# Kernel optimization log

Measured on AMD Instinct MI355X. Metric: run time of the kernel, lower is better.

The kernel has to match this reference:

```python
import jax, jax.numpy as jnp
import numpy as np

N_NODES = 100000
N_EDGES = 1200000
IN_F = 64
OUT_F = 64


def setup_inputs() -> dict:
    key = jax.random.key(0)
    ks = jax.random.split(key, 8)
    rows = jax.random.randint(ks[0], (N_EDGES,), 0, N_NODES)
    cols = jax.random.randint(ks[1], (N_EDGES,), 0, N_NODES)
    vals = jax.random.uniform(ks[2], (N_EDGES,), dtype=jnp.float32)
    features = jax.random.normal(ks[3], (N_NODES, IN_F), dtype=jnp.float32)
    W1 = jax.random.normal(ks[4], (IN_F, OUT_F), dtype=jnp.float32) / np.sqrt(IN_F)
    b1 = jax.random.normal(ks[5], (OUT_F,), dtype=jnp.float32) * 0.01
    W2 = jax.random.normal(ks[6], (IN_F, OUT_F), dtype=jnp.float32) / np.sqrt(IN_F)
    b2 = jax.random.normal(ks[7], (OUT_F,), dtype=jnp.float32) * 0.01
    return {"rows": rows, "cols": cols, "vals": vals, "features": features,
            "W1": W1, "b1": b1, "W2": W2, "b2": b2}


def _spmm(rows, cols, vals, x):
    # y[r] = sum_{e: rows[e]==r} vals[e] * x[cols[e]]  -- COO SpMM via gather + segment_sum
    msgs = vals[:, None] * x[cols]  # [E, F]
    return jax.ops.segment_sum(msgs, rows, num_segments=N_NODES)


def reference(rows, cols, vals, features, W1, b1, W2, b2):
    # L1 = laplacian + selfLoop(identity)  =>  L1 @ X = L @ X + X
    agg1 = _spmm(rows, cols, vals, features) + features          # [N, inF]
    inter_feature = features * features                           # elementwise square
    agg2 = _spmm(rows, cols, vals, inter_feature)                 # [N, inF]
    part1 = agg1 @ W1 + b1                                        # linear
    part2 = agg2 @ W2 + b2                                        # interActTransform
    return part1 + part2
```

## Files before the change

kernel.cpp:

```cpp
#include <hip/hip_runtime.h>


#define ROWS_PER_BUCKET 128
#define ROW_SHIFT 7
#define NBUCK_PAD 784
#define SCAN_T 196
#define CAP 2048
#define CHUNK 4096
#define MAXB 2048
#define COL_BITS 17
#define COL_MASK 0x1FFFF
#define OVF_CAP 65536

typedef __attribute__((ext_vector_type(8))) short bf16x8;
typedef __attribute__((ext_vector_type(4))) float f32x4;

__device__ __forceinline__ unsigned short f2bf(float x) {
    unsigned u = __float_as_uint(x);
    unsigned r = (u + 0x7FFFu + ((u >> 16) & 1u)) >> 16;
    return (unsigned short)r;
}
__device__ __forceinline__ float bf2f(unsigned short h) {
    return __uint_as_float(((unsigned)h) << 16);
}

__global__ __launch_bounds__(256) void node_transform(
    const float* __restrict__ X, const float* __restrict__ W1,
    const float* __restrict__ b1, const float* __restrict__ W2,
    const float* __restrict__ b2, unsigned short* __restrict__ Yb,
    float* __restrict__ Z, int n_nodes,
    int* __restrict__ gcursor, int* __restrict__ ovf_count)
{
    const int tid = threadIdx.x;

    if (gcursor) {
        int gi = blockIdx.x * 256 + tid;
        if (gi < NBUCK_PAD) gcursor[gi] = gi * CAP;
        if (gi == 0) *ovf_count = 0;
    }

    const int lane = tid & 63;
    const int wave = tid >> 6;
    const int lg = lane >> 4;
    const int lr = lane & 15;

    const int base = blockIdx.x * 128 + wave * 32;

    bf16x8 bw1[2][4];
    bf16x8 bw2[2][4];
#pragma unroll
    for (int ks = 0; ks < 2; ++ks) {
#pragma unroll
        for (int cf = 0; cf < 4; ++cf) {
            const int col = cf * 16 + lr;
            const int k0 = ks * 32 + lg * 8;
            bf16x8 t1, t2;
#pragma unroll
            for (int j = 0; j < 8; ++j) {
                t1[j] = (short)f2bf(W1[(k0 + j) * 64 + col]);
                t2[j] = (short)f2bf(W2[(k0 + j) * 64 + col]);
            }
            bw1[ks][cf] = t1;
            bw2[ks][cf] = t2;
        }
    }

    f32x4 acc1[2][4];
    f32x4 acc2[2][4];
#pragma unroll
    for (int rf = 0; rf < 2; ++rf)
#pragma unroll
        for (int cf = 0; cf < 4; ++cf) {
            acc1[rf][cf] = (f32x4){0.f, 0.f, 0.f, 0.f};
            acc2[rf][cf] = (f32x4){0.f, 0.f, 0.f, 0.f};
        }

#pragma unroll
    for (int rf = 0; rf < 2; ++rf) {
        const int row = base + rf * 16 + lr;
        const bool rok = row < n_nodes;
        const float* xp = X + (size_t)row * 64 + lg * 8;
#pragma unroll
        for (int ks = 0; ks < 2; ++ks) {
            float xv[8];
            if (rok) {
                float4 v0 = *(const float4*)(xp + ks * 32);
                float4 v1 = *(const float4*)(xp + ks * 32 + 4);
                xv[0] = v0.x; xv[1] = v0.y; xv[2] = v0.z; xv[3] = v0.w;
                xv[4] = v1.x; xv[5] = v1.y; xv[6] = v1.z; xv[7] = v1.w;
            } else {
#pragma unroll
                for (int j = 0; j < 8; ++j) xv[j] = 0.f;
            }
            bf16x8 a, q;
#pragma unroll
            for (int j = 0; j < 8; ++j) {
                a[j] = (short)f2bf(xv[j]);
                float s = xv[j] * xv[j];
                q[j] = (short)f2bf(s);
            }
#pragma unroll
            for (int cf = 0; cf < 4; ++cf) {
                acc1[rf][cf] = __builtin_amdgcn_mfma_f32_16x16x32_bf16(
                    a, bw1[ks][cf], acc1[rf][cf], 0, 0, 0);
                acc2[rf][cf] = __builtin_amdgcn_mfma_f32_16x16x32_bf16(
                    q, bw2[ks][cf], acc2[rf][cf], 0, 0, 0);
            }
        }
    }

    float bsv[4];
#pragma unroll
    for (int cf = 0; cf < 4; ++cf)
        bsv[cf] = b1[cf * 16 + lr] + b2[cf * 16 + lr];

#pragma unroll
    for (int rf = 0; rf < 2; ++rf) {
#pragma unroll
        for (int i = 0; i < 4; ++i) {
            const int row = base + rf * 16 + lg * 4 + i;
            if (row < n_nodes) {
#pragma unroll
                for (int cf = 0; cf < 4; ++cf) {
                    const float v1 = acc1[rf][cf][i];
                    const float y = v1 + acc2[rf][cf][i];
                    const float z = v1 + bsv[cf];
                    Yb[(size_t)row * 64 + cf * 16 + lr] = f2bf(y);
                    Z[(size_t)row * 64 + cf * 16 + lr] = z;
                }
            }
        }
    }
}


__global__ __launch_bounds__(256) void bin_scatter(
    const int* __restrict__ rows, const int* __restrict__ cols,
    const float* __restrict__ vals, int* __restrict__ gcursor,
    int2* __restrict__ packed, int* __restrict__ ovf_count,
    int4* __restrict__ ovf, int n_edges) {
    __shared__ int lcount[NBUCK_PAD];
    __shared__ int lstart[NBUCK_PAD];
    __shared__ int lcursor[NBUCK_PAD];
    __shared__ int gbase[NBUCK_PAD];
    __shared__ int sx[CHUNK];
    __shared__ int sy[CHUNK];
    __shared__ unsigned short sbk[CHUNK];

    int tid = threadIdx.x;
    int eb0 = blockIdx.x * CHUNK;
    int cnt = min(CHUNK, n_edges - eb0);

    for (int k = tid; k < NBUCK_PAD; k += 256) lcount[k] = 0;
    __syncthreads();

    for (int i = tid; i < cnt; i += 256)
        atomicAdd(&lcount[rows[eb0 + i] >> ROW_SHIFT], 1);
    __syncthreads();

    int c0 = 0, c1 = 0, c2 = 0, c3 = 0, psum = 0;
    if (tid < SCAN_T) {
        c0 = lcount[tid * 4 + 0]; c1 = lcount[tid * 4 + 1];
        c2 = lcount[tid * 4 + 2]; c3 = lcount[tid * 4 + 3];
        psum = c0 + c1 + c2 + c3;
    }
    sx[tid] = psum;
    __syncthreads();
#pragma unroll
    for (int o = 1; o < 256; o <<= 1) {
        int t = (tid >= o) ? sx[tid - o] : 0;
        __syncthreads();
        sx[tid] += t;
        __syncthreads();
    }
    int base0 = sx[tid] - psum;
    __syncthreads();
    if (tid < SCAN_T) {
        lstart[tid * 4 + 0] = base0;
        lstart[tid * 4 + 1] = base0 + c0;
        lstart[tid * 4 + 2] = base0 + c0 + c1;
        lstart[tid * 4 + 3] = base0 + c0 + c1 + c2;
    }
    __syncthreads();

    for (int k = tid; k < NBUCK_PAD; k += 256) {
        lcursor[k] = lstart[k];
        if (lcount[k] > 0) gbase[k] = atomicAdd(&gcursor[k], lcount[k]);
    }
    __syncthreads();

    for (int i = tid; i < cnt; i += 256) {
        int r = rows[eb0 + i];
        int b = r >> ROW_SHIFT;
        int p = atomicAdd(&lcursor[b], 1);
        sx[p] = ((r & (ROWS_PER_BUCKET - 1)) << COL_BITS) | cols[eb0 + i];
        sy[p] = __float_as_int(vals[eb0 + i]);
        sbk[p] = (unsigned short)b;
    }
    __syncthreads();

    for (int i = tid; i < cnt; i += 256) {
        int b = sbk[i];
        int dest = gbase[b] + (i - lstart[b]);
        if (dest < (b + 1) * CAP) {
            packed[dest] = make_int2(sx[i], sy[i]);
        } else {
            int p = atomicAdd(ovf_count, 1);
            if (p < OVF_CAP)
                ovf[p] = make_int4(b * ROWS_PER_BUCKET + (sx[i] >> COL_BITS),
                                   sx[i] & COL_MASK, sy[i], 0);
        }
    }
}

__global__ __launch_bounds__(256) void bucket_gather_quads(
    const int* __restrict__ gcursor, const int2* __restrict__ packed,
    const unsigned short* __restrict__ Yb, float* __restrict__ out,
    int n_nodes) {
    __shared__ int2 sxy[MAXB];
    __shared__ int hist[ROWS_PER_BUCKET];
    __shared__ int chs[ROWS_PER_BUCKET];
    __shared__ int chc[ROWS_PER_BUCKET];

    int tid = threadIdx.x;
    int bucket = blockIdx.x >> 1;
    int rhalf = (blockIdx.x & 1) * 64;
    int fquad = tid & 15;
    int grp = tid >> 4;
    int s = bucket * CAP;
    int e = min(gcursor[bucket], s + CAP);
    int row0 = bucket * ROWS_PER_BUCKET;
    const uint2* __restrict__ Y64 = (const uint2*)Yb;

    for (int cb = s; cb < e; cb += MAXB) {
        int cnt = min(MAXB, e - cb);

        if (tid < ROWS_PER_BUCKET) hist[tid] = 0;
        __syncthreads();

        for (int i = tid; i < cnt; i += 256)
            atomicAdd(&hist[packed[cb + i].x >> COL_BITS], 1);
        __syncthreads();

        if (tid < ROWS_PER_BUCKET) chs[tid] = hist[tid];
        __syncthreads();
#pragma unroll
        for (int o = 1; o < ROWS_PER_BUCKET; o <<= 1) {
            int t = 0;
            if (tid < ROWS_PER_BUCKET && tid >= o) t = chs[tid - o];
            __syncthreads();
            if (tid < ROWS_PER_BUCKET) chs[tid] += t;
            __syncthreads();
        }
        if (tid < ROWS_PER_BUCKET) {
            int excl = chs[tid] - hist[tid];
            chs[tid] = excl;
            chc[tid] = excl;
        }
        __syncthreads();

        for (int i = tid; i < cnt; i += 256) {
            int2 a = packed[cb + i];
            int p = atomicAdd(&chc[a.x >> COL_BITS], 1);
            sxy[p] = a;
        }
        __syncthreads();

        for (int rr = 0; rr < 4; ++rr) {
            int r = rhalf + grp * 4 + rr;
            int rc = hist[r];
            int node = row0 + r;
            if (rc == 0 || node >= n_nodes) continue;
            int rs = chs[r];
            float a0 = 0.f, a1 = 0.f, a2 = 0.f, a3 = 0.f;
            int j = 0;
            for (; j + 4 <= rc; j += 4) {
                int2 e0 = sxy[rs + j + 0], e1 = sxy[rs + j + 1];
                int2 e2 = sxy[rs + j + 2], e3 = sxy[rs + j + 3];
                uint2 u0 = Y64[(size_t)(e0.x & COL_MASK) * 16 + fquad];
                uint2 u1 = Y64[(size_t)(e1.x & COL_MASK) * 16 + fquad];
                uint2 u2 = Y64[(size_t)(e2.x & COL_MASK) * 16 + fquad];
                uint2 u3 = Y64[(size_t)(e3.x & COL_MASK) * 16 + fquad];
                float v0 = __int_as_float(e0.y), v1 = __int_as_float(e1.y);
                float v2 = __int_as_float(e2.y), v3 = __int_as_float(e3.y);
                a0 = fmaf(v0, __uint_as_float(u0.x << 16), a0);
                a1 = fmaf(v0, __uint_as_float(u0.x & 0xFFFF0000u), a1);
                a2 = fmaf(v0, __uint_as_float(u0.y << 16), a2);
                a3 = fmaf(v0, __uint_as_float(u0.y & 0xFFFF0000u), a3);
                a0 = fmaf(v1, __uint_as_float(u1.x << 16), a0);
                a1 = fmaf(v1, __uint_as_float(u1.x & 0xFFFF0000u), a1);
                a2 = fmaf(v1, __uint_as_float(u1.y << 16), a2);
                a3 = fmaf(v1, __uint_as_float(u1.y & 0xFFFF0000u), a3);
                a0 = fmaf(v2, __uint_as_float(u2.x << 16), a0);
                a1 = fmaf(v2, __uint_as_float(u2.x & 0xFFFF0000u), a1);
                a2 = fmaf(v2, __uint_as_float(u2.y << 16), a2);
                a3 = fmaf(v2, __uint_as_float(u2.y & 0xFFFF0000u), a3);
                a0 = fmaf(v3, __uint_as_float(u3.x << 16), a0);
                a1 = fmaf(v3, __uint_as_float(u3.x & 0xFFFF0000u), a1);
                a2 = fmaf(v3, __uint_as_float(u3.y << 16), a2);
                a3 = fmaf(v3, __uint_as_float(u3.y & 0xFFFF0000u), a3);
            }
            for (; j < rc; ++j) {
                int2 e0 = sxy[rs + j];
                uint2 u0 = Y64[(size_t)(e0.x & COL_MASK) * 16 + fquad];
                float v0 = __int_as_float(e0.y);
                a0 = fmaf(v0, __uint_as_float(u0.x << 16), a0);
                a1 = fmaf(v0, __uint_as_float(u0.x & 0xFFFF0000u), a1);
                a2 = fmaf(v0, __uint_as_float(u0.y << 16), a2);
                a3 = fmaf(v0, __uint_as_float(u0.y & 0xFFFF0000u), a3);
            }
            float4* op = (float4*)(out + (size_t)node * 64 + fquad * 4);
            float4 o = *op;
            o.x += a0; o.y += a1; o.z += a2; o.w += a3;
            *op = o;
        }
        __syncthreads();
    }
}

__global__ __launch_bounds__(256) void overflow_scatter(
    const int* __restrict__ ovf_count, const int4* __restrict__ ovf,
    const unsigned short* __restrict__ Yb, float* __restrict__ out) {
    int cnt = min(*ovf_count, OVF_CAP);
    long long total = (long long)cnt * 64;
    for (long long i = blockIdx.x * 256 + threadIdx.x; i < total;
         i += (long long)gridDim.x * 256) {
        int e = (int)(i >> 6), f = (int)(i & 63);
        int4 a = ovf[e];
        atomicAdd(&out[(size_t)a.x * 64 + f],
                  __int_as_float(a.z) * bf2f(Yb[(size_t)a.y * 64 + f]));
    }
}


__global__ __launch_bounds__(256) void edge_scatter(
    const int* __restrict__ rows, const int* __restrict__ cols,
    const float* __restrict__ vals, const unsigned short* __restrict__ Yb,
    float* __restrict__ out, int n_edges)
{
    int t = blockIdx.x * 256 + threadIdx.x;
    int e = t >> 4;
    int f = (t & 15) << 2;
    if (e >= n_edges) return;
    int r = rows[e];
    int c = cols[e];
    float v = vals[e];
    const unsigned short* y = Yb + (size_t)c * 64 + f;
    float* o = out + (size_t)r * 64 + f;
    atomicAdd(o + 0, v * bf2f(y[0]));
    atomicAdd(o + 1, v * bf2f(y[1]));
    atomicAdd(o + 2, v * bf2f(y[2]));
    atomicAdd(o + 3, v * bf2f(y[3]));
}

extern "C" void kernel_launch(void* const* d_in, const int* in_sizes, int n_in,
                              void* d_out, int out_size, void* d_ws, size_t ws_size,
                              hipStream_t stream) {
    const int*   rows = (const int*)d_in[0];
    const int*   cols = (const int*)d_in[1];
    const float* vals = (const float*)d_in[2];
    const float* X    = (const float*)d_in[3];
    const float* W1   = (const float*)d_in[4];
    const float* b1   = (const float*)d_in[5];
    const float* W2   = (const float*)d_in[6];
    const float* b2   = (const float*)d_in[7];
    float* out = (float*)d_out;

    const int n_edges = in_sizes[0];
    const int n_nodes = in_sizes[3] / 64;
    const int nbuck = (n_nodes + ROWS_PER_BUCKET - 1) / ROWS_PER_BUCKET;

    char* ws = (char*)d_ws;
    size_t o_Yb     = 0;
    size_t o_packed = o_Yb + (size_t)n_nodes * 64 * 2;
    size_t o_ovf    = o_packed + (size_t)NBUCK_PAD * CAP * 8;
    size_t o_gcurs  = o_ovf + (size_t)OVF_CAP * 16;
    size_t o_ovfcnt = o_gcurs + NBUCK_PAD * 4;
    size_t need     = o_ovfcnt + 16;

    unsigned short* Yb = (unsigned short*)(ws + o_Yb);

    const bool fastpath =
        ws_size >= need && nbuck <= NBUCK_PAD && n_nodes <= (1 << COL_BITS);

    int2* packed  = (int2*)(ws + o_packed);
    int4* ovf     = (int4*)(ws + o_ovf);
    int*  gcursor = fastpath ? (int*)(ws + o_gcurs) : (int*)0;
    int*  ovfcnt  = (int*)(ws + o_ovfcnt);

    int nblocks = (n_nodes + 127) / 128;
    node_transform<<<nblocks, 256, 0, stream>>>(X, W1, b1, W2, b2, Yb, out,
                                                n_nodes, gcursor, ovfcnt);

    if (fastpath) {
        int eb = (n_edges + CHUNK - 1) / CHUNK;
        bin_scatter<<<eb, 256, 0, stream>>>(rows, cols, vals, gcursor, packed,
                                            ovfcnt, ovf, n_edges);
        bucket_gather_quads<<<nbuck * 2, 256, 0, stream>>>(gcursor, packed, Yb,
                                                           out, n_nodes);
        overflow_scatter<<<128, 256, 0, stream>>>(ovfcnt, ovf, Yb, out);
    } else {
        long long threads = (long long)n_edges * 16;
        int eblocks = (int)((threads + 255) / 256);
        edge_scatter<<<eblocks, 256, 0, stream>>>(rows, cols, vals, Yb, out, n_edges);
    }
}
```

Before: 173.7 us.

## Replace block-local bucket binning with per-edge global atomics on padded cursors

The shared-memory counting sort in the binning kernel (local histogram, scan, staging, then coalesced write-out) is replaced by a one-thread-per-edge kernel. Each thread takes its slot with a global atomicAdd on a bucket cursor, and cursors are padded to a 128-byte stride to avoid false sharing. This drops the block-level scans and barriers, but puts about 1.2M global atomics on 782 addresses and scatters uncoalesced 8-byte writes. Edge order within a bucket becomes nondeterministic, which changes floating-point summation order.

```diff
diff --git a/kernel.cpp b/kernel.cpp
--- a/kernel.cpp
+++ b/kernel.cpp
@@ -4,10 +4,9 @@
 #define ROWS_PER_BUCKET 128
 #define ROW_SHIFT 7
 #define NBUCK_PAD 784
-#define SCAN_T 196
 #define CAP 2048
-#define CHUNK 4096
 #define MAXB 2048
+#define GC_STRIDE 32
 #define COL_BITS 17
 #define COL_MASK 0x1FFFF
 #define OVF_CAP 65536
@@ -35,7 +34,7 @@
 
     if (gcursor) {
         int gi = blockIdx.x * 256 + tid;
-        if (gi < NBUCK_PAD) gcursor[gi] = gi * CAP;
+        if (gi < NBUCK_PAD) gcursor[(size_t)gi * GC_STRIDE] = gi * CAP;
         if (gi == 0) *ovf_count = 0;
     }
 
@@ -134,82 +133,25 @@
 }
 
 
-__global__ __launch_bounds__(256) void bin_scatter(
+__global__ __launch_bounds__(256) void bin_scatter_direct(
     const int* __restrict__ rows, const int* __restrict__ cols,
     const float* __restrict__ vals, int* __restrict__ gcursor,
     int2* __restrict__ packed, int* __restrict__ ovf_count,
     int4* __restrict__ ovf, int n_edges) {
-    __shared__ int lcount[NBUCK_PAD];
-    __shared__ int lstart[NBUCK_PAD];
-    __shared__ int lcursor[NBUCK_PAD];
-    __shared__ int gbase[NBUCK_PAD];
-    __shared__ int sx[CHUNK];
-    __shared__ int sy[CHUNK];
-    __shared__ unsigned short sbk[CHUNK];
-
-    int tid = threadIdx.x;
-    int eb0 = blockIdx.x * CHUNK;
-    int cnt = min(CHUNK, n_edges - eb0);
-
-    for (int k = tid; k < NBUCK_PAD; k += 256) lcount[k] = 0;
-    __syncthreads();
-
-    for (int i = tid; i < cnt; i += 256)
-        atomicAdd(&lcount[rows[eb0 + i] >> ROW_SHIFT], 1);
-    __syncthreads();
-
-    int c0 = 0, c1 = 0, c2 = 0, c3 = 0, psum = 0;
-    if (tid < SCAN_T) {
-        c0 = lcount[tid * 4 + 0]; c1 = lcount[tid * 4 + 1];
-        c2 = lcount[tid * 4 + 2]; c3 = lcount[tid * 4 + 3];
-        psum = c0 + c1 + c2 + c3;
-    }
-    sx[tid] = psum;
-    __syncthreads();
-#pragma unroll
-    for (int o = 1; o < 256; o <<= 1) {
-        int t = (tid >= o) ? sx[tid - o] : 0;
-        __syncthreads();
-        sx[tid] += t;
-        __syncthreads();
-    }
-    int base0 = sx[tid] - psum;
-    __syncthreads();
-    if (tid < SCAN_T) {
-        lstart[tid * 4 + 0] = base0;
-        lstart[tid * 4 + 1] = base0 + c0;
-        lstart[tid * 4 + 2] = base0 + c0 + c1;
-        lstart[tid * 4 + 3] = base0 + c0 + c1 + c2;
-    }
-    __syncthreads();
-
-    for (int k = tid; k < NBUCK_PAD; k += 256) {
-        lcursor[k] = lstart[k];
-        if (lcount[k] > 0) gbase[k] = atomicAdd(&gcursor[k], lcount[k]);
-    }
-    __syncthreads();
-
-    for (int i = tid; i < cnt; i += 256) {
-        int r = rows[eb0 + i];
-        int b = r >> ROW_SHIFT;
-        int p = atomicAdd(&lcursor[b], 1);
-        sx[p] = ((r & (ROWS_PER_BUCKET - 1)) << COL_BITS) | cols[eb0 + i];
-        sy[p] = __float_as_int(vals[eb0 + i]);
-        sbk[p] = (unsigned short)b;
-    }
-    __syncthreads();
-
-    for (int i = tid; i < cnt; i += 256) {
-        int b = sbk[i];
-        int dest = gbase[b] + (i - lstart[b]);
-        if (dest < (b + 1) * CAP) {
-            packed[dest] = make_int2(sx[i], sy[i]);
-        } else {
-            int p = atomicAdd(ovf_count, 1);
-            if (p < OVF_CAP)
-                ovf[p] = make_int4(b * ROWS_PER_BUCKET + (sx[i] >> COL_BITS),
-                                   sx[i] & COL_MASK, sy[i], 0);
-        }
+    int i = blockIdx.x * 256 + threadIdx.x;
+    if (i >= n_edges) return;
+    int r = rows[i];
+    int c = cols[i];
+    float v = vals[i];
+    int b = r >> ROW_SHIFT;
+    int x = ((r & (ROWS_PER_BUCKET - 1)) << COL_BITS) | c;
+    int dest = atomicAdd(&gcursor[(size_t)b * GC_STRIDE], 1);
+    if (dest < (b + 1) * CAP) {
+        packed[dest] = make_int2(x, __float_as_int(v));
+    } else {
+        int p = atomicAdd(ovf_count, 1);
+        if (p < OVF_CAP)
+            ovf[p] = make_int4(r, c, __float_as_int(v), 0);
     }
 }
 
@@ -228,7 +170,7 @@
     int fquad = tid & 15;
     int grp = tid >> 4;
     int s = bucket * CAP;
-    int e = min(gcursor[bucket], s + CAP);
+    int e = min(gcursor[(size_t)bucket * GC_STRIDE], s + CAP);
     int row0 = bucket * ROWS_PER_BUCKET;
     const uint2* __restrict__ Y64 = (const uint2*)Yb;
 
@@ -375,7 +317,7 @@
     size_t o_packed = o_Yb + (size_t)n_nodes * 64 * 2;
     size_t o_ovf    = o_packed + (size_t)NBUCK_PAD * CAP * 8;
     size_t o_gcurs  = o_ovf + (size_t)OVF_CAP * 16;
-    size_t o_ovfcnt = o_gcurs + NBUCK_PAD * 4;
+    size_t o_ovfcnt = o_gcurs + (size_t)NBUCK_PAD * GC_STRIDE * 4;
     size_t need     = o_ovfcnt + 16;
 
     unsigned short* Yb = (unsigned short*)(ws + o_Yb);
@@ -393,9 +335,9 @@
                                                 n_nodes, gcursor, ovfcnt);
 
     if (fastpath) {
-        int eb = (n_edges + CHUNK - 1) / CHUNK;
-        bin_scatter<<<eb, 256, 0, stream>>>(rows, cols, vals, gcursor, packed,
-                                            ovfcnt, ovf, n_edges);
+        int eb = (n_edges + 255) / 256;
+        bin_scatter_direct<<<eb, 256, 0, stream>>>(rows, cols, vals, gcursor,
+                                                   packed, ovfcnt, ovf, n_edges);
         bucket_gather_quads<<<nbuck * 2, 256, 0, stream>>>(gcursor, packed, Yb,
                                                            out, n_nodes);
         overflow_scatter<<<128, 256, 0, stream>>>(ovfcnt, ovf, Yb, out);
```

After: 210.3 us. 21.1% more time.

## Keep edge data in registers across bin_scatter passes and use wave-shuffle scan

Applied to the files above, without the earlier changes.

The bin_scatter kernel now reads rows, cols and vals once into per-thread register arrays (16 edges per thread). The atomic return value from the counting pass becomes each edge's local rank, so the second global read and the second shared-memory atomic pass over lcursor go away. The 256-step shared-memory Hillis-Steele scan with a barrier per step is replaced by a wavefront shuffle scan plus a small cross-wave combine. Shared x/y arrays are merged into an int2 array. This raises register pressure (64 extra registers per thread) and drops one barrier before the scatter.

```diff
diff --git a/kernel.cpp b/kernel.cpp
--- a/kernel.cpp
+++ b/kernel.cpp
@@ -7,6 +7,7 @@
 #define SCAN_T 196
 #define CAP 2048
 #define CHUNK 4096
+#define EPT 16
 #define MAXB 2048
 #define COL_BITS 17
 #define COL_MASK 0x1FFFF
@@ -141,11 +142,10 @@
     int4* __restrict__ ovf, int n_edges) {
     __shared__ int lcount[NBUCK_PAD];
     __shared__ int lstart[NBUCK_PAD];
-    __shared__ int lcursor[NBUCK_PAD];
     __shared__ int gbase[NBUCK_PAD];
-    __shared__ int sx[CHUNK];
-    __shared__ int sy[CHUNK];
+    __shared__ int2 sxy[CHUNK];
     __shared__ unsigned short sbk[CHUNK];
+    __shared__ int wsum[4];
 
     int tid = threadIdx.x;
     int eb0 = blockIdx.x * CHUNK;
@@ -154,8 +154,21 @@
     for (int k = tid; k < NBUCK_PAD; k += 256) lcount[k] = 0;
     __syncthreads();
 
-    for (int i = tid; i < cnt; i += 256)
-        atomicAdd(&lcount[rows[eb0 + i] >> ROW_SHIFT], 1);
+    int eb_[EPT], ep_[EPT], ex_[EPT], ey_[EPT];
+#pragma unroll
+    for (int t = 0; t < EPT; ++t) {
+        int i = tid + 256 * t;
+        if (i < cnt) {
+            int r = rows[eb0 + i];
+            int b = r >> ROW_SHIFT;
+            eb_[t] = b;
+            ep_[t] = atomicAdd(&lcount[b], 1);
+            ex_[t] = ((r & (ROWS_PER_BUCKET - 1)) << COL_BITS) | cols[eb0 + i];
+            ey_[t] = __float_as_int(vals[eb0 + i]);
+        } else {
+            eb_[t] = -1; ep_[t] = 0; ex_[t] = 0; ey_[t] = 0;
+        }
+    }
     __syncthreads();
 
     int c0 = 0, c1 = 0, c2 = 0, c3 = 0, psum = 0;
@@ -164,17 +177,21 @@
         c2 = lcount[tid * 4 + 2]; c3 = lcount[tid * 4 + 3];
         psum = c0 + c1 + c2 + c3;
     }
-    sx[tid] = psum;
+    const int lane = tid & 63;
+    const int wv = tid >> 6;
+    int incl = psum;
+#pragma unroll
+    for (int o = 1; o < 64; o <<= 1) {
+        int n = __shfl_up(incl, o);
+        if (lane >= o) incl += n;
+    }
+    if (lane == 63) wsum[wv] = incl;
     __syncthreads();
-#pragma unroll
-    for (int o = 1; o < 256; o <<= 1) {
-        int t = (tid >= o) ? sx[tid - o] : 0;
-        __syncthreads();
-        sx[tid] += t;
-        __syncthreads();
-    }
-    int base0 = sx[tid] - psum;
-    __syncthreads();
+    int wpre = 0;
+#pragma unroll
+    for (int w = 0; w < 3; ++w)
+        if (w < wv) wpre += wsum[w];
+    int base0 = wpre + incl - psum;
     if (tid < SCAN_T) {
         lstart[tid * 4 + 0] = base0;
         lstart[tid * 4 + 1] = base0 + c0;
@@ -184,31 +201,30 @@
     __syncthreads();
 
     for (int k = tid; k < NBUCK_PAD; k += 256) {
-        lcursor[k] = lstart[k];
         if (lcount[k] > 0) gbase[k] = atomicAdd(&gcursor[k], lcount[k]);
     }
-    __syncthreads();
-
-    for (int i = tid; i < cnt; i += 256) {
-        int r = rows[eb0 + i];
-        int b = r >> ROW_SHIFT;
-        int p = atomicAdd(&lcursor[b], 1);
-        sx[p] = ((r & (ROWS_PER_BUCKET - 1)) << COL_BITS) | cols[eb0 + i];
-        sy[p] = __float_as_int(vals[eb0 + i]);
-        sbk[p] = (unsigned short)b;
+
+#pragma unroll
+    for (int t = 0; t < EPT; ++t) {
+        if (eb_[t] >= 0) {
+            int p = lstart[eb_[t]] + ep_[t];
+            sxy[p] = make_int2(ex_[t], ey_[t]);
+            sbk[p] = (unsigned short)eb_[t];
+        }
     }
     __syncthreads();
 
     for (int i = tid; i < cnt; i += 256) {
         int b = sbk[i];
+        int2 a = sxy[i];
         int dest = gbase[b] + (i - lstart[b]);
         if (dest < (b + 1) * CAP) {
-            packed[dest] = make_int2(sx[i], sy[i]);
+            packed[dest] = a;
         } else {
             int p = atomicAdd(ovf_count, 1);
             if (p < OVF_CAP)
-                ovf[p] = make_int4(b * ROWS_PER_BUCKET + (sx[i] >> COL_BITS),
-                                   sx[i] & COL_MASK, sy[i], 0);
+                ovf[p] = make_int4(b * ROWS_PER_BUCKET + (a.x >> COL_BITS),
+                                   a.x & COL_MASK, a.y, 0);
         }
     }
 }
```

Result: faster. 160.8 us (-7.4%).
